# Performance work log

Measured on AMD Instinct MI355X. Metric: run time of the kernel, lower is better.

The kernel has to match this reference:

```python
import jax, jax.numpy as jnp
import numpy as np

N = 100000
E = 1600000
F_IN = 128
HID = 32
HEADS = 4
NCLS = 64
NEG_SLOPE = 0.2
EPS = 1e-16


def setup_inputs() -> dict:
    key = jax.random.key(0)
    ks = jax.random.split(key, 12)
    inp = jax.random.normal(ks[0], (N, F_IN), dtype=jnp.float32)
    edge_index = jax.random.randint(ks[1], (2, E), 0, N, dtype=jnp.int64)
    s1 = 1.0 / np.sqrt(F_IN)
    W1 = jax.random.uniform(ks[2], (F_IN, HEADS, HID), jnp.float32, -s1, s1)
    att_src1 = jax.random.normal(ks[3], (HEADS, HID), dtype=jnp.float32) * s1
    att_dst1 = jax.random.normal(ks[4], (HEADS, HID), dtype=jnp.float32) * s1
    bias1 = jnp.zeros((HEADS * HID,), dtype=jnp.float32)
    d2 = HEADS * HID
    s2 = 1.0 / np.sqrt(d2)
    W2 = jax.random.uniform(ks[5], (d2, 1, NCLS), jnp.float32, -s2, s2)
    att_src2 = jax.random.normal(ks[6], (1, NCLS), dtype=jnp.float32) * s2
    att_dst2 = jax.random.normal(ks[7], (1, NCLS), dtype=jnp.float32) * s2
    bias2 = jnp.zeros((NCLS,), dtype=jnp.float32)
    return {"inp": inp, "edge_index": edge_index, "W1": W1, "att_src1": att_src1,
            "att_dst1": att_dst1, "bias1": bias1, "W2": W2, "att_src2": att_src2,
            "att_dst2": att_dst2, "bias2": bias2}


def _gat_layer(x, src, dst, W, a_src, a_dst, bias):
    # x: [N, F]; W: [F, H, C]
    h = jnp.einsum('nf,fhc->nhc', x, W)            # [N, H, C]
    a_s = jnp.sum(h * a_src[None], axis=-1)        # [N, H]
    a_d = jnp.sum(h * a_dst[None], axis=-1)        # [N, H]
    e = a_s[src] + a_d[dst]                        # [Etot, H]
    e = jnp.where(e >= 0, e, NEG_SLOPE * e)        # LeakyReLU(0.2)
    # softmax normalized per destination node (segment softmax)
    m = jax.ops.segment_max(e, dst, num_segments=N)      # [N, H]
    ex = jnp.exp(e - m[dst])
    denom = jax.ops.segment_sum(ex, dst, num_segments=N)  # [N, H]
    alpha = ex / (denom[dst] + EPS)                # [Etot, H]
    msg = h[src] * alpha[..., None]                # [Etot, H, C]
    out = jax.ops.segment_sum(msg, dst, num_segments=N)   # [N, H, C]
    return out.reshape(N, -1) + bias


def reference(inp, edge_index, W1, att_src1, att_dst1, bias1, W2, att_src2, att_dst2, bias2):
    # add self-loops (PyG GATConv default)
    loop = jnp.arange(N, dtype=edge_index.dtype)
    src = jnp.concatenate([edge_index[0], loop])
    dst = jnp.concatenate([edge_index[1], loop])
    x = _gat_layer(inp, src, dst, W1, att_src1, att_dst1, bias1)   # [N, H*HID]
    x = _gat_layer(x, src, dst, W2, att_src2, att_dst2, bias2)     # [N, NCLS]
    return x
```

## Files before the change

### kernel.cpp

```cpp
#include <hip/hip_runtime.h>

#define N_NODES 100000
#define F1 128
#define NCLS 64
#define EPB 8
#define BCAP 12288

typedef __attribute__((ext_vector_type(8))) short bf16x8;
typedef __attribute__((ext_vector_type(4))) float f32x4;

__device__ __forceinline__ unsigned f2bf(float x) {
    unsigned u = __builtin_bit_cast(unsigned, x);
    u += 0x7fff + ((u >> 16) & 1);
    return u >> 16;
}
__device__ __forceinline__ float bflo(unsigned u) {
    return __builtin_bit_cast(float, u << 16);
}
__device__ __forceinline__ float bfhi(unsigned u) {
    return __builtin_bit_cast(float, u & 0xffff0000u);
}

#define SWZ_I(v, off) __builtin_amdgcn_ds_swizzle((v), (off))
#define SWZ_F(v, off) __builtin_bit_cast(float, __builtin_amdgcn_ds_swizzle(__builtin_bit_cast(int, (v)), (off)))

__device__ __forceinline__ int load_edge(const int* ei, int is64, long long idx) {
    return is64 ? ei[2 * idx] : ei[idx];
}

#define EDGE_PROBE(ei, s_is64, tid) { \
    int v_ = (ei)[2 * ((tid) & 63) + 1]; \
    unsigned long long b_ = __ballot(v_ == 0); \
    if ((tid) == 0) s_is64 = (b_ == ~0ull) ? 1 : 0; }

#define BSUM_SCAN(sm, bsum, nb, tid) { \
    sm[tid] = ((tid) < (nb)) ? bsum[tid] : 0; \
    __syncthreads(); \
    for (int off_ = 1; off_ < 256; off_ <<= 1) { \
        int t_ = ((tid) >= off_) ? sm[(tid) - off_] : 0; \
        __syncthreads(); \
        sm[tid] += t_; \
        __syncthreads(); \
    } }

__global__ __launch_bounds__(256) void histgemm1_kernel(
        const int* __restrict__ ei, int* __restrict__ ghBM, int EB, int E,
        const float* __restrict__ x, const float* __restrict__ W,
        const float* __restrict__ att_s, const float* __restrict__ att_d,
        unsigned* __restrict__ hp, float* __restrict__ as_, float* __restrict__ ad_, int n) {
    __shared__ uint4 WtS[2048];
    __shared__ int s_is64;
    int tid = threadIdx.x;
    if (blockIdx.x < (unsigned)EB) {
        int* bins = (int*)WtS;
        bins[tid] = 0;
        EDGE_PROBE(ei, s_is64, tid)
        __syncthreads();
        int is64 = s_is64;
        long long base = (long long)blockIdx.x * 2048 + tid * EPB;
        int d[EPB];
        #pragma unroll
        for (int k = 0; k < EPB; ++k) {
            long long e = base + k;
            d[k] = (e < E) ? load_edge(ei, is64, (long long)E + e) : -1;
        }
        #pragma unroll
        for (int k = 0; k < EPB; ++k)
            if (d[k] >= 0) atomicAdd(&bins[d[k] >> 9], 1);
        __syncthreads();
        ghBM[(size_t)tid * EB + blockIdx.x] = bins[tid];
        return;
    }
    unsigned* Wt = (unsigned*)WtS;
    {
        int ch = tid & 127, fb = tid >> 7;
        #pragma unroll
        for (int j8 = 0; j8 < 8; ++j8) {
            int f0 = fb * 64 + j8 * 8;
            unsigned pk[4];
            #pragma unroll
            for (int p = 0; p < 4; ++p) {
                float lo = W[(size_t)(f0 + 2 * p) * 128 + ch];
                float hi = W[(size_t)(f0 + 2 * p + 1) * 128 + ch];
                pk[p] = f2bf(lo) | (f2bf(hi) << 16);
            }
            int bcol = (f0 * 2) ^ ((ch & 7) << 4);
            *(uint4*)&Wt[ch * 64 + (bcol >> 2)] = *(uint4*)pk;
        }
    }
    __syncthreads();
    int lane = tid & 63, w = tid >> 6;
    int col = lane & 15, quad = lane >> 4;
    int nodebase = (blockIdx.x - EB) * 128 + w * 32;
    bf16x8 a[2][4];
    #pragma unroll
    for (int s = 0; s < 2; ++s) {
        int node = nodebase + s * 16 + col;
        const float* xr = x + (size_t)node * 128;
        bool v = node < n;
        #pragma unroll
        for (int kk = 0; kk < 4; ++kk) {
            float4 lo = v ? *(const float4*)&xr[kk * 32 + quad * 8]
                          : make_float4(0.f, 0.f, 0.f, 0.f);
            float4 hi = v ? *(const float4*)&xr[kk * 32 + quad * 8 + 4]
                          : make_float4(0.f, 0.f, 0.f, 0.f);
            unsigned pk[4];
            pk[0] = f2bf(lo.x) | (f2bf(lo.y) << 16);
            pk[1] = f2bf(lo.z) | (f2bf(lo.w) << 16);
            pk[2] = f2bf(hi.x) | (f2bf(hi.y) << 16);
            pk[3] = f2bf(hi.z) | (f2bf(hi.w) << 16);
            a[s][kk] = *(bf16x8*)pk;
        }
    }
    f32x4 acc[2][8] = {};
    #pragma unroll
    for (int c = 0; c < 8; ++c) {
        int brow = c * 16 + col;
        bf16x8 b[4];
        #pragma unroll
        for (int kk = 0; kk < 4; ++kk) {
            int bcol = (kk * 64 + quad * 16) ^ ((brow & 7) << 4);
            b[kk] = *(bf16x8*)&Wt[brow * 64 + (bcol >> 2)];
        }
        #pragma unroll
        for (int s = 0; s < 2; ++s)
            #pragma unroll
            for (int kk = 0; kk < 4; ++kk)
                acc[s][c] = __builtin_amdgcn_mfma_f32_16x16x32_bf16(a[s][kk], b[kk], acc[s][c], 0, 0, 0);
    }
    float aS[8], aD[8];
    #pragma unroll
    for (int c = 0; c < 8; ++c) { aS[c] = att_s[c * 16 + col]; aD[c] = att_d[c * 16 + col]; }
    #pragma unroll
    for (int s = 0; s < 2; ++s) {
        #pragma unroll
        for (int c = 0; c < 8; ++c) {
            #pragma unroll
            for (int r = 0; r < 4; ++r) {
                float own = acc[s][c][r];
                float par = SWZ_F(own, 0x041F);
                int node = nodebase + s * 16 + quad * 4 + r;
                if (!(lane & 1) && node < n)
                    hp[(size_t)node * 64 + c * 8 + (col >> 1)] =
                        f2bf(own) | (f2bf(par) << 16);
            }
        }
        #pragma unroll
        for (int h = 0; h < 4; ++h) {
            #pragma unroll
            for (int r = 0; r < 4; ++r) {
                float ps = acc[s][2 * h][r] * aS[2 * h] + acc[s][2 * h + 1][r] * aS[2 * h + 1];
                float pd = acc[s][2 * h][r] * aD[2 * h] + acc[s][2 * h + 1][r] * aD[2 * h + 1];
                ps += SWZ_F(ps, 0x041F); pd += SWZ_F(pd, 0x041F);
                ps += SWZ_F(ps, 0x081F); pd += SWZ_F(pd, 0x081F);
                ps += SWZ_F(ps, 0x101F); pd += SWZ_F(pd, 0x101F);
                ps += SWZ_F(ps, 0x201F); pd += SWZ_F(pd, 0x201F);
                int node = nodebase + s * 16 + quad * 4 + r;
                if (col == 0 && node < n) {
                    as_[(size_t)node * 4 + h] = ps;
                    ad_[(size_t)node * 4 + h] = pd;
                }
            }
        }
    }
}

#define SCAN_BLOCK 1024
__global__ void pscanA_kernel(int* __restrict__ g, int* __restrict__ bsum, int K) {
    __shared__ int sm[SCAN_BLOCK];
    int tid = threadIdx.x;
    int i = blockIdx.x * SCAN_BLOCK + tid;
    int v = (i < K) ? g[i] : 0;
    sm[tid] = v;
    __syncthreads();
    for (int off = 1; off < SCAN_BLOCK; off <<= 1) {
        int t = (tid >= off) ? sm[tid - off] : 0;
        __syncthreads();
        sm[tid] += t;
        __syncthreads();
    }
    if (i < K) g[i] = sm[tid] - v;
    if (tid == SCAN_BLOCK - 1) bsum[blockIdx.x] = sm[tid];
}

__global__ __launch_bounds__(256) void scatterB_kernel(
        const int* __restrict__ ei, const int* __restrict__ ghBM, int EB,
        const int* __restrict__ bsum, int nbK,
        unsigned* __restrict__ tmp, int E) {
    __shared__ int base[256];
    __shared__ int sm[256];
    __shared__ int s_is64;
    int tid = threadIdx.x;
    EDGE_PROBE(ei, s_is64, tid)
    BSUM_SCAN(sm, bsum, nbK, tid)
    {
        int idx = tid * EB + blockIdx.x;
        int chunk = idx >> 10;
        int pre = (chunk == 0) ? 0 : sm[chunk - 1];
        base[tid] = ghBM[(size_t)idx] + pre;
    }
    __syncthreads();
    int is64 = s_is64;
    long long eb = (long long)blockIdx.x * 2048 + tid * EPB;
    int d[EPB], s[EPB];
    #pragma unroll
    for (int k = 0; k < EPB; ++k) {
        long long e = eb + k;
        d[k] = (e < E) ? load_edge(ei, is64, (long long)E + e) : -1;
    }
    #pragma unroll
    for (int k = 0; k < EPB; ++k) {
        long long e = eb + k;
        s[k] = (e < E) ? load_edge(ei, is64, e) : 0;
    }
    #pragma unroll
    for (int k = 0; k < EPB; ++k) {
        if (d[k] >= 0) {
            int pos = atomicAdd(&base[d[k] >> 9], 1);
            tmp[pos] = (unsigned)s[k] | ((unsigned)(d[k] & 511) << 17);
        }
    }
}

__global__ __launch_bounds__(256) void bucketC_kernel(
        const unsigned* __restrict__ tmp, const int* __restrict__ ghBM, int EB,
        const int* __restrict__ bsum, int nbK,
        int* __restrict__ row_ptr, int* __restrict__ col, int E, int n) {
    __shared__ unsigned stmp[BCAP];
    __shared__ int lb[512];
    __shared__ int lo[512];
    __shared__ int sm[256];
    int bk = blockIdx.x;
    int tid = threadIdx.x;
    BSUM_SCAN(sm, bsum, nbK, tid)
    int i0 = bk * EB;
    int c0 = (i0 >> 10), p0 = (c0 == 0) ? 0 : sm[c0 - 1];
    int gbase = ghBM[(size_t)i0] + p0;
    int gend = E;
    if (bk < 255) {
        int i1 = (bk + 1) * EB;
        int c1 = (i1 >> 10), p1 = (c1 == 0) ? 0 : sm[c1 - 1];
        gend = ghBM[(size_t)i1] + p1;
    }
    int cnt = gend - gbase;
    bool lds = (cnt <= BCAP);
    __syncthreads();
    lb[tid] = 0; lb[tid + 256] = 0;
    if (lds) {
        for (int i = tid; i < cnt; i += 256) stmp[i] = tmp[gbase + i];
    }
    __syncthreads();
    if (lds) {
        for (int i = tid; i < cnt; i += 256)
            atomicAdd(&lb[stmp[i] >> 17], 1);
    } else {
        for (int i = tid; i < cnt; i += 256)
            atomicAdd(&lb[tmp[gbase + i] >> 17], 1);
    }
    __syncthreads();
    int p = lb[2 * tid], q = lb[2 * tid + 1];
    int ps = p + q;
    sm[tid] = ps;
    __syncthreads();
    for (int off = 1; off < 256; off <<= 1) {
        int t = (tid >= off) ? sm[tid - off] : 0;
        __syncthreads();
        sm[tid] += t;
        __syncthreads();
    }
    int excl = sm[tid] - ps;
    int e0 = excl, e1 = excl + p;
    lo[2 * tid] = e0; lo[2 * tid + 1] = e1;
    int v0 = bk * 512 + 2 * tid;
    if (v0 <= n) row_ptr[v0] = gbase + e0;
    if (v0 + 1 <= n) row_ptr[v0 + 1] = gbase + e1;
    __syncthreads();
    if (lds) {
        for (int i = tid; i < cnt; i += 256) {
            unsigned v = stmp[i];
            int r = atomicAdd(&lo[v >> 17], 1);
            col[gbase + r] = (int)(v & 0x1FFFFu);
        }
    } else {
        for (int i = tid; i < cnt; i += 256) {
            unsigned v = tmp[gbase + i];
            int r = atomicAdd(&lo[v >> 17], 1);
            col[gbase + r] = (int)(v & 0x1FFFFu);
        }
    }
}

__global__ __launch_bounds__(256) void gemm2_kernel(
        const unsigned* __restrict__ xp, const float* __restrict__ W,
        const float* __restrict__ att_s, const float* __restrict__ att_d,
        unsigned* __restrict__ hp, float* __restrict__ as_, float* __restrict__ ad_, int n) {
    __shared__ uint4 WtS[1024];
    unsigned* Wt = (unsigned*)WtS;
    int tid = threadIdx.x;
    {
        int ch = tid & 63, fb = tid >> 6;
        #pragma unroll
        for (int j8 = 0; j8 < 4; ++j8) {
            int f0 = fb * 32 + j8 * 8;
            unsigned pk[4];
            #pragma unroll
            for (int p = 0; p < 4; ++p) {
                float lo = W[(size_t)(f0 + 2 * p) * 64 + ch];
                float hi = W[(size_t)(f0 + 2 * p + 1) * 64 + ch];
                pk[p] = f2bf(lo) | (f2bf(hi) << 16);
            }
            int bcol = (f0 * 2) ^ ((ch & 7) << 4);
            *(uint4*)&Wt[ch * 64 + (bcol >> 2)] = *(uint4*)pk;
        }
    }
    __syncthreads();
    int lane = tid & 63, w = tid >> 6;
    int col = lane & 15, quad = lane >> 4;
    int nodebase = blockIdx.x * 128 + w * 32;
    bf16x8 a[2][4];
    #pragma unroll
    for (int s = 0; s < 2; ++s) {
        int node = nodebase + s * 16 + col;
        bool v = node < n;
        #pragma unroll
        for (int kk = 0; kk < 4; ++kk) {
            uint4 u = v ? *(const uint4*)&xp[(size_t)node * 64 + kk * 16 + quad * 4]
                        : make_uint4(0, 0, 0, 0);
            a[s][kk] = *(bf16x8*)&u;
        }
    }
    f32x4 acc[2][4] = {};
    #pragma unroll
    for (int c = 0; c < 4; ++c) {
        int brow = c * 16 + col;
        bf16x8 b[4];
        #pragma unroll
        for (int kk = 0; kk < 4; ++kk) {
            int bcol = (kk * 64 + quad * 16) ^ ((brow & 7) << 4);
            b[kk] = *(bf16x8*)&Wt[brow * 64 + (bcol >> 2)];
        }
        #pragma unroll
        for (int s = 0; s < 2; ++s)
            #pragma unroll
            for (int kk = 0; kk < 4; ++kk)
                acc[s][c] = __builtin_amdgcn_mfma_f32_16x16x32_bf16(a[s][kk], b[kk], acc[s][c], 0, 0, 0);
    }
    float aS[4], aD[4];
    #pragma unroll
    for (int c = 0; c < 4; ++c) { aS[c] = att_s[c * 16 + col]; aD[c] = att_d[c * 16 + col]; }
    #pragma unroll
    for (int s = 0; s < 2; ++s) {
        #pragma unroll
        for (int c = 0; c < 4; ++c) {
            #pragma unroll
            for (int r = 0; r < 4; ++r) {
                float own = acc[s][c][r];
                float par = SWZ_F(own, 0x041F);
                int node = nodebase + s * 16 + quad * 4 + r;
                if (!(lane & 1) && node < n)
                    hp[(size_t)node * 32 + c * 8 + (col >> 1)] =
                        f2bf(own) | (f2bf(par) << 16);
            }
        }
        #pragma unroll
        for (int r = 0; r < 4; ++r) {
            float ps = 0.f, pd = 0.f;
            #pragma unroll
            for (int c = 0; c < 4; ++c) {
                ps = fmaf(acc[s][c][r], aS[c], ps);
                pd = fmaf(acc[s][c][r], aD[c], pd);
            }
            ps += SWZ_F(ps, 0x041F); pd += SWZ_F(pd, 0x041F);
            ps += SWZ_F(ps, 0x081F); pd += SWZ_F(pd, 0x081F);
            ps += SWZ_F(ps, 0x101F); pd += SWZ_F(pd, 0x101F);
            ps += SWZ_F(ps, 0x201F); pd += SWZ_F(pd, 0x201F);
            int node = nodebase + s * 16 + quad * 4 + r;
            if (col == 0 && node < n) { as_[node] = ps; ad_[node] = pd; }
        }
    }
}

#define A1_G8(B, K0) { \
    int t0 = SWZ_I(myc, (((B)+(K0)+0)<<5)); \
    int t1 = SWZ_I(myc, (((B)+(K0)+1)<<5)); \
    int t2 = SWZ_I(myc, (((B)+(K0)+2)<<5)); \
    int t3 = SWZ_I(myc, (((B)+(K0)+3)<<5)); \
    int t4 = SWZ_I(myc, (((B)+(K0)+4)<<5)); \
    int t5 = SWZ_I(myc, (((B)+(K0)+5)<<5)); \
    int t6 = SWZ_I(myc, (((B)+(K0)+6)<<5)); \
    int t7 = SWZ_I(myc, (((B)+(K0)+7)<<5)); \
    unsigned v0 = hp[(size_t)t0 * 64 + lane]; \
    unsigned v1 = hp[(size_t)t1 * 64 + lane]; \
    unsigned v2 = hp[(size_t)t2 * 64 + lane]; \
    unsigned v3 = hp[(size_t)t3 * 64 + lane]; \
    unsigned v4 = hp[(size_t)t4 * 64 + lane]; \
    unsigned v5 = hp[(size_t)t5 * 64 + lane]; \
    unsigned v6 = hp[(size_t)t6 * 64 + lane]; \
    unsigned v7 = hp[(size_t)t7 * 64 + lane]; \
    float q0 = SWZ_F(ew, ((((K0)+0)<<5)|0x10)); \
    float q1 = SWZ_F(ew, ((((K0)+1)<<5)|0x10)); \
    float q2 = SWZ_F(ew, ((((K0)+2)<<5)|0x10)); \
    float q3 = SWZ_F(ew, ((((K0)+3)<<5)|0x10)); \
    float q4 = SWZ_F(ew, ((((K0)+4)<<5)|0x10)); \
    float q5 = SWZ_F(ew, ((((K0)+5)<<5)|0x10)); \
    float q6 = SWZ_F(ew, ((((K0)+6)<<5)|0x10)); \
    float q7 = SWZ_F(ew, ((((K0)+7)<<5)|0x10)); \
    s += q0; acc0 = fmaf(q0, bflo(v0), acc0); acc1 = fmaf(q0, bfhi(v0), acc1); \
    s += q1; acc0 = fmaf(q1, bflo(v1), acc0); acc1 = fmaf(q1, bfhi(v1), acc1); \
    s += q2; acc0 = fmaf(q2, bflo(v2), acc0); acc1 = fmaf(q2, bfhi(v2), acc1); \
    s += q3; acc0 = fmaf(q3, bflo(v3), acc0); acc1 = fmaf(q3, bfhi(v3), acc1); \
    s += q4; acc0 = fmaf(q4, bflo(v4), acc0); acc1 = fmaf(q4, bfhi(v4), acc1); \
    s += q5; acc0 = fmaf(q5, bflo(v5), acc0); acc1 = fmaf(q5, bfhi(v5), acc1); \
    s += q6; acc0 = fmaf(q6, bflo(v6), acc0); acc1 = fmaf(q6, bfhi(v6), acc1); \
    s += q7; acc0 = fmaf(q7, bflo(v7), acc0); acc1 = fmaf(q7, bfhi(v7), acc1); }

#define A1_SUB(B) { \
    int sspec = SWZ_I(myc, (((B)<<5) | 0x0F)); \
    float ee_ = as_[(size_t)sspec * 4 + head] + adv; \
    ee_ = fmaxf(ee_, 0.2f * ee_); \
    float ew = ((cb + (B) + (lane & 15)) < end) ? __expf(ee_) : 0.f; \
    A1_G8(B, 0) \
    if (m > (B) + 8) A1_G8(B, 8) }

__global__ __launch_bounds__(256) void agg1_kernel(
        const unsigned* __restrict__ hp, const float* __restrict__ as_,
        const float* __restrict__ ad_, const int* __restrict__ row_ptr,
        const int* __restrict__ col, const float* __restrict__ bias,
        unsigned* __restrict__ outp, int n) {
    int wid = (blockIdx.x * 256 + threadIdx.x) >> 6;
    int lane = threadIdx.x & 63;
    if (wid >= n) return;
    int node = wid;
    int head = lane >> 4;
    float adv = ad_[(size_t)node * 4 + head];
    float e0 = as_[(size_t)node * 4 + head] + adv;
    e0 = fmaxf(e0, 0.2f * e0);
    float w0 = __expf(e0);
    float s = w0;
    unsigned u0 = hp[(size_t)node * 64 + lane];
    float acc0 = w0 * bflo(u0), acc1 = w0 * bfhi(u0);
    int beg = row_ptr[node], end = row_ptr[node + 1];
    for (int cb = beg; cb < end; cb += 32) {
        int m = end - cb; if (m > 32) m = 32;
        int ci = cb + (lane & 31);
        int myc = col[(ci < end) ? ci : (end - 1)];
        A1_SUB(0)
        if (m > 16) A1_SUB(16)
    }
    float inv = 1.0f / (s + 1e-16f);
    float2 b = *(const float2*)&bias[lane * 2];
    outp[(size_t)node * 64 + lane] =
        f2bf(acc0 * inv + b.x) | (f2bf(acc1 * inv + b.y) << 16);
}

#define A2_G4(K0) { \
    int t0 = SWZ_I(myc, (((K0)+0)<<5)); \
    int t1 = SWZ_I(myc, (((K0)+1)<<5)); \
    int t2 = SWZ_I(myc, (((K0)+2)<<5)); \
    int t3 = SWZ_I(myc, (((K0)+3)<<5)); \
    unsigned v0 = hp[(size_t)t0 * 32 + wrd]; \
    unsigned v1 = hp[(size_t)t1 * 32 + wrd]; \
    unsigned v2 = hp[(size_t)t2 * 32 + wrd]; \
    unsigned v3 = hp[(size_t)t3 * 32 + wrd]; \
    float q0 = SWZ_F(ew, (((K0)+0)<<5)); \
    float q1 = SWZ_F(ew, (((K0)+1)<<5)); \
    float q2 = SWZ_F(ew, (((K0)+2)<<5)); \
    float q3 = SWZ_F(ew, (((K0)+3)<<5)); \
    s += q0; acc0 = fmaf(q0, bflo(v0), acc0); acc1 = fmaf(q0, bfhi(v0), acc1); \
    s += q1; acc0 = fmaf(q1, bflo(v1), acc0); acc1 = fmaf(q1, bfhi(v1), acc1); \
    s += q2; acc0 = fmaf(q2, bflo(v2), acc0); acc1 = fmaf(q2, bfhi(v2), acc1); \
    s += q3; acc0 = fmaf(q3, bflo(v3), acc0); acc1 = fmaf(q3, bfhi(v3), acc1); }

__global__ __launch_bounds__(256) void agg2_kernel(
        const unsigned* __restrict__ hp, const float* __restrict__ as_,
        const float* __restrict__ ad_, const int* __restrict__ row_ptr,
        const int* __restrict__ col, const float* __restrict__ bias,
        float* __restrict__ out, int n) {
    int wid = (blockIdx.x * 256 + threadIdx.x) >> 6;
    int lane = threadIdx.x & 63;
    if (wid >= n) return;
    int node = wid;
    int half = lane >> 5, wrd = lane & 31;
    float adv = ad_[node];
    float s = 0.f, acc0 = 0.f, acc1 = 0.f;
    {
        float e = as_[node] + adv; e = fmaxf(e, 0.2f * e);
        float w = __expf(e);
        if (half == 0) {
            unsigned u = hp[(size_t)node * 32 + wrd];
            s = w; acc0 = w * bflo(u); acc1 = w * bfhi(u);
        }
    }
    int beg = row_ptr[node], end = row_ptr[node + 1];
    for (int cb = beg; cb < end; cb += 64) {
        int m = end - cb; if (m > 64) m = 64;
        int idx = cb + 2 * (lane & 31) + half;
        int myc = col[(idx < end) ? idx : (end - 1)];
        float ee = as_[myc] + adv; ee = fmaxf(ee, 0.2f * ee);
        float ew = (idx < end) ? __expf(ee) : 0.f;
        A2_G4(0)
        if (m > 8)  A2_G4(4)
        if (m > 16) A2_G4(8)
        if (m > 24) A2_G4(12)
        if (m > 32) {
            A2_G4(16)
            if (m > 40) A2_G4(20)
            if (m > 48) A2_G4(24)
            if (m > 56) A2_G4(28)
        }
    }
    s += __shfl_xor(s, 32);
    acc0 += __shfl_xor(acc0, 32);
    acc1 += __shfl_xor(acc1, 32);
    if (half == 0) {
        float inv = 1.0f / (s + 1e-16f);
        float2 b = *(const float2*)&bias[wrd * 2];
        *(float2*)&out[(size_t)node * 64 + wrd * 2] =
            make_float2(acc0 * inv + b.x, acc1 * inv + b.y);
    }
}

extern "C" void kernel_launch(void* const* d_in, const int* in_sizes, int n_in,
                              void* d_out, int out_size, void* d_ws, size_t ws_size,
                              hipStream_t stream) {
    const float* inp   = (const float*)d_in[0];
    const int*   ei    = (const int*)d_in[1];
    const float* W1    = (const float*)d_in[2];
    const float* atts1 = (const float*)d_in[3];
    const float* attd1 = (const float*)d_in[4];
    const float* bias1 = (const float*)d_in[5];
    const float* W2    = (const float*)d_in[6];
    const float* atts2 = (const float*)d_in[7];
    const float* attd2 = (const float*)d_in[8];
    const float* bias2 = (const float*)d_in[9];
    float* out = (float*)d_out;

    const int N = N_NODES;
    const int E = in_sizes[1] / 2;

    const int EB = (E + 2047) / 2048;
    const int K = 256 * EB;
    const int nbK = (K + SCAN_BLOCK - 1) / SCAN_BLOCK;
    const int nG1 = (N + 127) / 128;

    unsigned* h1p = (unsigned*)d_ws;
    unsigned* x1p = h1p + (size_t)N * 64;
    float* as1 = (float*)(x1p + (size_t)N * 64);
    float* ad1 = as1 + (size_t)N * 4;
    int* row_ptr  = (int*)(ad1 + (size_t)N * 4);
    int* col      = row_ptr + N + 1;
    int* ghBM     = col + E;
    int* bsum     = ghBM + K;
    unsigned* tmp = x1p;

    histgemm1_kernel<<<EB + nG1, 256, 0, stream>>>(
        ei, ghBM, EB, E, inp, W1, atts1, attd1, h1p, as1, ad1, N);
    pscanA_kernel<<<nbK, SCAN_BLOCK, 0, stream>>>(ghBM, bsum, K);
    scatterB_kernel<<<EB, 256, 0, stream>>>(ei, ghBM, EB, bsum, nbK, tmp, E);
    bucketC_kernel<<<256, 256, 0, stream>>>(tmp, ghBM, EB, bsum, nbK, row_ptr, col, E, N);

    agg1_kernel<<<(N + 3) / 4, 256, 0, stream>>>(h1p, as1, ad1, row_ptr, col, bias1, x1p, N);

    gemm2_kernel<<<(N + 127) / 128, 256, 0, stream>>>(x1p, W2, atts2, attd2, h1p, as1, ad1, N);
    agg2_kernel<<<(N + 3) / 4, 256, 0, stream>>>(h1p, as1, ad1, row_ptr, col, bias2, out, N);
}
```

Measured before the change: 204.7 us.

## Gather neighbour features with 8-byte loads and split edges across lane groups

Both aggregation kernels now have each lane load 8 bytes (4 bf16 features) per neighbour instead of 4 bytes. Each wave processes several neighbours in parallel: two in layer 1, four in layer 2. Partial sums are combined with cross-lane shuffles at the end. The aim is fewer, wider gather transactions and more memory-level parallelism per wave. In exchange, ds_swizzle is replaced by __shfl (ds_bpermute) broadcasts, extra reductions are added, and layer 2 uses coarser predication granularity.

```diff
diff --git a/kernel.cpp b/kernel.cpp
--- a/kernel.cpp
+++ b/kernel.cpp
@@ -380,47 +380,51 @@
     }
 }
 
-#define A1_G8(B, K0) { \
-    int t0 = SWZ_I(myc, (((B)+(K0)+0)<<5)); \
-    int t1 = SWZ_I(myc, (((B)+(K0)+1)<<5)); \
-    int t2 = SWZ_I(myc, (((B)+(K0)+2)<<5)); \
-    int t3 = SWZ_I(myc, (((B)+(K0)+3)<<5)); \
-    int t4 = SWZ_I(myc, (((B)+(K0)+4)<<5)); \
-    int t5 = SWZ_I(myc, (((B)+(K0)+5)<<5)); \
-    int t6 = SWZ_I(myc, (((B)+(K0)+6)<<5)); \
-    int t7 = SWZ_I(myc, (((B)+(K0)+7)<<5)); \
-    unsigned v0 = hp[(size_t)t0 * 64 + lane]; \
-    unsigned v1 = hp[(size_t)t1 * 64 + lane]; \
-    unsigned v2 = hp[(size_t)t2 * 64 + lane]; \
-    unsigned v3 = hp[(size_t)t3 * 64 + lane]; \
-    unsigned v4 = hp[(size_t)t4 * 64 + lane]; \
-    unsigned v5 = hp[(size_t)t5 * 64 + lane]; \
-    unsigned v6 = hp[(size_t)t6 * 64 + lane]; \
-    unsigned v7 = hp[(size_t)t7 * 64 + lane]; \
-    float q0 = SWZ_F(ew, ((((K0)+0)<<5)|0x10)); \
-    float q1 = SWZ_F(ew, ((((K0)+1)<<5)|0x10)); \
-    float q2 = SWZ_F(ew, ((((K0)+2)<<5)|0x10)); \
-    float q3 = SWZ_F(ew, ((((K0)+3)<<5)|0x10)); \
-    float q4 = SWZ_F(ew, ((((K0)+4)<<5)|0x10)); \
-    float q5 = SWZ_F(ew, ((((K0)+5)<<5)|0x10)); \
-    float q6 = SWZ_F(ew, ((((K0)+6)<<5)|0x10)); \
-    float q7 = SWZ_F(ew, ((((K0)+7)<<5)|0x10)); \
-    s += q0; acc0 = fmaf(q0, bflo(v0), acc0); acc1 = fmaf(q0, bfhi(v0), acc1); \
-    s += q1; acc0 = fmaf(q1, bflo(v1), acc0); acc1 = fmaf(q1, bfhi(v1), acc1); \
-    s += q2; acc0 = fmaf(q2, bflo(v2), acc0); acc1 = fmaf(q2, bfhi(v2), acc1); \
-    s += q3; acc0 = fmaf(q3, bflo(v3), acc0); acc1 = fmaf(q3, bfhi(v3), acc1); \
-    s += q4; acc0 = fmaf(q4, bflo(v4), acc0); acc1 = fmaf(q4, bfhi(v4), acc1); \
-    s += q5; acc0 = fmaf(q5, bflo(v5), acc0); acc1 = fmaf(q5, bfhi(v5), acc1); \
-    s += q6; acc0 = fmaf(q6, bflo(v6), acc0); acc1 = fmaf(q6, bfhi(v6), acc1); \
-    s += q7; acc0 = fmaf(q7, bflo(v7), acc0); acc1 = fmaf(q7, bfhi(v7), acc1); }
-
-#define A1_SUB(B) { \
-    int sspec = SWZ_I(myc, (((B)<<5) | 0x0F)); \
-    float ee_ = as_[(size_t)sspec * 4 + head] + adv; \
+#define A1N_SUB(B) { \
+    int sspec = __shfl(myc, (B) + (lane & 15)); \
+    float ee_ = as_[(size_t)sspec * 4 + heads] + adv_s; \
     ee_ = fmaxf(ee_, 0.2f * ee_); \
     float ew = ((cb + (B) + (lane & 15)) < end) ? __expf(ee_) : 0.f; \
-    A1_G8(B, 0) \
-    if (m > (B) + 8) A1_G8(B, 8) }
+    int s0 = __shfl(myc, (B) + 0 + h); \
+    int s1 = __shfl(myc, (B) + 2 + h); \
+    int s2 = __shfl(myc, (B) + 4 + h); \
+    int s3 = __shfl(myc, (B) + 6 + h); \
+    int s4 = __shfl(myc, (B) + 8 + h); \
+    int s5 = __shfl(myc, (B) + 10 + h); \
+    int s6 = __shfl(myc, (B) + 12 + h); \
+    int s7 = __shfl(myc, (B) + 14 + h); \
+    uint2 v0 = *(const uint2*)&hp[(size_t)s0 * 64 + c * 2]; \
+    uint2 v1 = *(const uint2*)&hp[(size_t)s1 * 64 + c * 2]; \
+    uint2 v2 = *(const uint2*)&hp[(size_t)s2 * 64 + c * 2]; \
+    uint2 v3 = *(const uint2*)&hp[(size_t)s3 * 64 + c * 2]; \
+    uint2 v4 = *(const uint2*)&hp[(size_t)s4 * 64 + c * 2]; \
+    uint2 v5 = *(const uint2*)&hp[(size_t)s5 * 64 + c * 2]; \
+    uint2 v6 = *(const uint2*)&hp[(size_t)s6 * 64 + c * 2]; \
+    uint2 v7 = *(const uint2*)&hp[(size_t)s7 * 64 + c * 2]; \
+    float q0 = __shfl(ew, wbase + 0); \
+    float q1 = __shfl(ew, wbase + 2); \
+    float q2 = __shfl(ew, wbase + 4); \
+    float q3 = __shfl(ew, wbase + 6); \
+    float q4 = __shfl(ew, wbase + 8); \
+    float q5 = __shfl(ew, wbase + 10); \
+    float q6 = __shfl(ew, wbase + 12); \
+    float q7 = __shfl(ew, wbase + 14); \
+    s += q0; a0 = fmaf(q0, bflo(v0.x), a0); a1 = fmaf(q0, bfhi(v0.x), a1); \
+             a2 = fmaf(q0, bflo(v0.y), a2); a3 = fmaf(q0, bfhi(v0.y), a3); \
+    s += q1; a0 = fmaf(q1, bflo(v1.x), a0); a1 = fmaf(q1, bfhi(v1.x), a1); \
+             a2 = fmaf(q1, bflo(v1.y), a2); a3 = fmaf(q1, bfhi(v1.y), a3); \
+    s += q2; a0 = fmaf(q2, bflo(v2.x), a0); a1 = fmaf(q2, bfhi(v2.x), a1); \
+             a2 = fmaf(q2, bflo(v2.y), a2); a3 = fmaf(q2, bfhi(v2.y), a3); \
+    s += q3; a0 = fmaf(q3, bflo(v3.x), a0); a1 = fmaf(q3, bfhi(v3.x), a1); \
+             a2 = fmaf(q3, bflo(v3.y), a2); a3 = fmaf(q3, bfhi(v3.y), a3); \
+    s += q4; a0 = fmaf(q4, bflo(v4.x), a0); a1 = fmaf(q4, bfhi(v4.x), a1); \
+             a2 = fmaf(q4, bflo(v4.y), a2); a3 = fmaf(q4, bfhi(v4.y), a3); \
+    s += q5; a0 = fmaf(q5, bflo(v5.x), a0); a1 = fmaf(q5, bfhi(v5.x), a1); \
+             a2 = fmaf(q5, bflo(v5.y), a2); a3 = fmaf(q5, bfhi(v5.y), a3); \
+    s += q6; a0 = fmaf(q6, bflo(v6.x), a0); a1 = fmaf(q6, bfhi(v6.x), a1); \
+             a2 = fmaf(q6, bflo(v6.y), a2); a3 = fmaf(q6, bfhi(v6.y), a3); \
+    s += q7; a0 = fmaf(q7, bflo(v7.x), a0); a1 = fmaf(q7, bfhi(v7.x), a1); \
+             a2 = fmaf(q7, bflo(v7.y), a2); a3 = fmaf(q7, bfhi(v7.y), a3); }
 
 __global__ __launch_bounds__(256) void agg1_kernel(
         const unsigned* __restrict__ hp, const float* __restrict__ as_,
@@ -431,45 +435,66 @@
     int lane = threadIdx.x & 63;
     if (wid >= n) return;
     int node = wid;
-    int head = lane >> 4;
-    float adv = ad_[(size_t)node * 4 + head];
-    float e0 = as_[(size_t)node * 4 + head] + adv;
-    e0 = fmaxf(e0, 0.2f * e0);
-    float w0 = __expf(e0);
-    float s = w0;
-    unsigned u0 = hp[(size_t)node * 64 + lane];
-    float acc0 = w0 * bflo(u0), acc1 = w0 * bfhi(u0);
+    int h = lane >> 5;
+    int c = lane & 31;
+    int headc = c >> 3;
+    int heads = lane >> 4;
+    int wbase = h + (headc << 4);
+    float adv_c = ad_[(size_t)node * 4 + headc];
+    float adv_s = ad_[(size_t)node * 4 + heads];
+    float s, a0, a1, a2, a3;
+    {
+        float e0 = as_[(size_t)node * 4 + headc] + adv_c;
+        e0 = fmaxf(e0, 0.2f * e0);
+        float w0 = (h == 0) ? __expf(e0) : 0.f;
+        uint2 u = *(const uint2*)&hp[(size_t)node * 64 + c * 2];
+        s = w0;
+        a0 = w0 * bflo(u.x); a1 = w0 * bfhi(u.x);
+        a2 = w0 * bflo(u.y); a3 = w0 * bfhi(u.y);
+    }
     int beg = row_ptr[node], end = row_ptr[node + 1];
     for (int cb = beg; cb < end; cb += 32) {
         int m = end - cb; if (m > 32) m = 32;
-        int ci = cb + (lane & 31);
+        int ci = cb + c;
         int myc = col[(ci < end) ? ci : (end - 1)];
-        A1_SUB(0)
-        if (m > 16) A1_SUB(16)
-    }
-    float inv = 1.0f / (s + 1e-16f);
-    float2 b = *(const float2*)&bias[lane * 2];
-    outp[(size_t)node * 64 + lane] =
-        f2bf(acc0 * inv + b.x) | (f2bf(acc1 * inv + b.y) << 16);
-}
-
-#define A2_G4(K0) { \
-    int t0 = SWZ_I(myc, (((K0)+0)<<5)); \
-    int t1 = SWZ_I(myc, (((K0)+1)<<5)); \
-    int t2 = SWZ_I(myc, (((K0)+2)<<5)); \
-    int t3 = SWZ_I(myc, (((K0)+3)<<5)); \
-    unsigned v0 = hp[(size_t)t0 * 32 + wrd]; \
-    unsigned v1 = hp[(size_t)t1 * 32 + wrd]; \
-    unsigned v2 = hp[(size_t)t2 * 32 + wrd]; \
-    unsigned v3 = hp[(size_t)t3 * 32 + wrd]; \
-    float q0 = SWZ_F(ew, (((K0)+0)<<5)); \
-    float q1 = SWZ_F(ew, (((K0)+1)<<5)); \
-    float q2 = SWZ_F(ew, (((K0)+2)<<5)); \
-    float q3 = SWZ_F(ew, (((K0)+3)<<5)); \
-    s += q0; acc0 = fmaf(q0, bflo(v0), acc0); acc1 = fmaf(q0, bfhi(v0), acc1); \
-    s += q1; acc0 = fmaf(q1, bflo(v1), acc0); acc1 = fmaf(q1, bfhi(v1), acc1); \
-    s += q2; acc0 = fmaf(q2, bflo(v2), acc0); acc1 = fmaf(q2, bfhi(v2), acc1); \
-    s += q3; acc0 = fmaf(q3, bflo(v3), acc0); acc1 = fmaf(q3, bfhi(v3), acc1); }
+        A1N_SUB(0)
+        if (m > 16) A1N_SUB(16)
+    }
+    s  += __shfl_xor(s, 32);
+    a0 += __shfl_xor(a0, 32); a1 += __shfl_xor(a1, 32);
+    a2 += __shfl_xor(a2, 32); a3 += __shfl_xor(a3, 32);
+    if (h == 0) {
+        float inv = 1.0f / (s + 1e-16f);
+        float4 b = *(const float4*)&bias[c * 4];
+        uint2 o;
+        o.x = f2bf(a0 * inv + b.x) | (f2bf(a1 * inv + b.y) << 16);
+        o.y = f2bf(a2 * inv + b.z) | (f2bf(a3 * inv + b.w) << 16);
+        *(uint2*)&outp[(size_t)node * 64 + c * 2] = o;
+    }
+}
+
+#define A2N_G4(K0) { \
+    int i0 = 4 * (K0) + g; \
+    int s0 = __shfl(myc, i0); \
+    int s1 = __shfl(myc, i0 + 4); \
+    int s2 = __shfl(myc, i0 + 8); \
+    int s3 = __shfl(myc, i0 + 12); \
+    uint2 v0 = *(const uint2*)&hp[(size_t)s0 * 32 + w16 * 2]; \
+    uint2 v1 = *(const uint2*)&hp[(size_t)s1 * 32 + w16 * 2]; \
+    uint2 v2 = *(const uint2*)&hp[(size_t)s2 * 32 + w16 * 2]; \
+    uint2 v3 = *(const uint2*)&hp[(size_t)s3 * 32 + w16 * 2]; \
+    float q0 = __shfl(ewl, i0); \
+    float q1 = __shfl(ewl, i0 + 4); \
+    float q2 = __shfl(ewl, i0 + 8); \
+    float q3 = __shfl(ewl, i0 + 12); \
+    s += q0; a0 = fmaf(q0, bflo(v0.x), a0); a1 = fmaf(q0, bfhi(v0.x), a1); \
+             a2 = fmaf(q0, bflo(v0.y), a2); a3 = fmaf(q0, bfhi(v0.y), a3); \
+    s += q1; a0 = fmaf(q1, bflo(v1.x), a0); a1 = fmaf(q1, bfhi(v1.x), a1); \
+             a2 = fmaf(q1, bflo(v1.y), a2); a3 = fmaf(q1, bfhi(v1.y), a3); \
+    s += q2; a0 = fmaf(q2, bflo(v2.x), a0); a1 = fmaf(q2, bfhi(v2.x), a1); \
+             a2 = fmaf(q2, bflo(v2.y), a2); a3 = fmaf(q2, bfhi(v2.y), a3); \
+    s += q3; a0 = fmaf(q3, bflo(v3.x), a0); a1 = fmaf(q3, bfhi(v3.x), a1); \
+             a2 = fmaf(q3, bflo(v3.y), a2); a3 = fmaf(q3, bfhi(v3.y), a3); }
 
 __global__ __launch_bounds__(256) void agg2_kernel(
         const unsigned* __restrict__ hp, const float* __restrict__ as_,
@@ -480,43 +505,41 @@
     int lane = threadIdx.x & 63;
     if (wid >= n) return;
     int node = wid;
-    int half = lane >> 5, wrd = lane & 31;
+    int g = lane >> 4;
+    int w16 = lane & 15;
     float adv = ad_[node];
-    float s = 0.f, acc0 = 0.f, acc1 = 0.f;
+    float s, a0, a1, a2, a3;
     {
         float e = as_[node] + adv; e = fmaxf(e, 0.2f * e);
-        float w = __expf(e);
-        if (half == 0) {
-            unsigned u = hp[(size_t)node * 32 + wrd];
-            s = w; acc0 = w * bflo(u); acc1 = w * bfhi(u);
-        }
+        float w = (g == 0) ? __expf(e) : 0.f;
+        uint2 u = *(const uint2*)&hp[(size_t)node * 32 + w16 * 2];
+        s = w;
+        a0 = w * bflo(u.x); a1 = w * bfhi(u.x);
+        a2 = w * bflo(u.y); a3 = w * bfhi(u.y);
     }
     int beg = row_ptr[node], end = row_ptr[node + 1];
     for (int cb = beg; cb < end; cb += 64) {
         int m = end - cb; if (m > 64) m = 64;
-        int idx = cb + 2 * (lane & 31) + half;
-        int myc = col[(idx < end) ? idx : (end - 1)];
+        int ci = cb + lane;
+        int myc = col[(ci < end) ? ci : (end - 1)];
         float ee = as_[myc] + adv; ee = fmaxf(ee, 0.2f * ee);
-        float ew = (idx < end) ? __expf(ee) : 0.f;
-        A2_G4(0)
-        if (m > 8)  A2_G4(4)
-        if (m > 16) A2_G4(8)
-        if (m > 24) A2_G4(12)
-        if (m > 32) {
-            A2_G4(16)
-            if (m > 40) A2_G4(20)
-            if (m > 48) A2_G4(24)
-            if (m > 56) A2_G4(28)
-        }
-    }
-    s += __shfl_xor(s, 32);
-    acc0 += __shfl_xor(acc0, 32);
-    acc1 += __shfl_xor(acc1, 32);
-    if (half == 0) {
+        float ewl = (ci < end) ? __expf(ee) : 0.f;
+        A2N_G4(0)
+        if (m > 16) A2N_G4(4)
+        if (m > 32) A2N_G4(8)
+        if (m > 48) A2N_G4(12)
+    }
+    s  += __shfl_xor(s, 16);  s  += __shfl_xor(s, 32);
+    a0 += __shfl_xor(a0, 16); a0 += __shfl_xor(a0, 32);
+    a1 += __shfl_xor(a1, 16); a1 += __shfl_xor(a1, 32);
+    a2 += __shfl_xor(a2, 16); a2 += __shfl_xor(a2, 32);
+    a3 += __shfl_xor(a3, 16); a3 += __shfl_xor(a3, 32);
+    if (lane < 16) {
         float inv = 1.0f / (s + 1e-16f);
-        float2 b = *(const float2*)&bias[wrd * 2];
-        *(float2*)&out[(size_t)node * 64 + wrd * 2] =
-            make_float2(acc0 * inv + b.x, acc1 * inv + b.y);
+        float4 b = *(const float4*)&bias[w16 * 4];
+        *(float4*)&out[(size_t)node * 64 + w16 * 4] =
+            make_float4(a0 * inv + b.x, a1 * inv + b.y,
+                        a2 * inv + b.z, a3 * inv + b.w);
     }
 }
 
```

Result: no change. 206.2 us (+0.8%).
